# Optimization experiments

Measured on AMD Instinct MI355X. Metric: run time of the kernel, lower is better.

The kernel has to match this reference:

```python
import jax, jax.numpy as jnp
import numpy as np

BLOCK = 128  # fp8 block-quant block size (128, 128)


def dequant_block_fp8_weight(w, scale_inv):
    """w: [O, I] fp8-valued weights (stored as f32); scale_inv: [O//128, I//128].
    Dequant = per-(128,128)-block multiply by scale."""
    O, I = w.shape
    wb = w.reshape(O // BLOCK, BLOCK, I // BLOCK, BLOCK)
    wb = wb * scale_inv[:, None, :, None]
    return wb.reshape(O, I)


def setup_inputs() -> dict:
    key = jax.random.key(0)
    ks = jax.random.split(key, 7)
    H, F, T = 5120, 1536, 8192  # hidden, moe_intermediate, tokens
    x = jax.random.normal(ks[0], (T, H), dtype=jnp.float32)
    w_gate = jax.random.normal(ks[1], (F, H), dtype=jnp.float32)
    s_gate = jax.random.uniform(ks[2], (F // BLOCK, H // BLOCK), dtype=jnp.float32) * 0.01 + 1e-4
    w_up = jax.random.normal(ks[3], (F, H), dtype=jnp.float32)
    s_up = jax.random.uniform(ks[4], (F // BLOCK, H // BLOCK), dtype=jnp.float32) * 0.01 + 1e-4
    w_down = jax.random.normal(ks[5], (H, F), dtype=jnp.float32)
    s_down = jax.random.uniform(ks[6], (H // BLOCK, F // BLOCK), dtype=jnp.float32) * 0.01 + 1e-4
    return {"x": x, "w_gate": w_gate, "s_gate": s_gate, "w_up": w_up,
            "s_up": s_up, "w_down": w_down, "s_down": s_down}


def reference(x, w_gate, s_gate, w_up, s_up, w_down, s_down):
    # down_proj(silu(gate_proj(x)) * up_proj(x)), each Linear dequantizing
    # block-scaled fp8 weights first (bias=False everywhere).
    wg = dequant_block_fp8_weight(w_gate, s_gate).astype(x.dtype)
    wu = dequant_block_fp8_weight(w_up, s_up).astype(x.dtype)
    wd = dequant_block_fp8_weight(w_down, s_down).astype(x.dtype)
    gate = jnp.einsum('th,fh->tf', x, wg)  # [T, F]
    up = jnp.einsum('th,fh->tf', x, wu)    # [T, F]
    h = jax.nn.silu(gate) * up
    out = jnp.einsum('tf,hf->th', h, wd)   # [T, H]
    return out
```

## Files before the change

kernel.cpp:

```cpp
#include <hip/hip_runtime.h>


typedef __bf16 bf16x8 __attribute__((ext_vector_type(8)));
typedef float  f32x4  __attribute__((ext_vector_type(4)));
typedef unsigned int u32x4 __attribute__((ext_vector_type(4)));

__device__ __forceinline__ void glds16(const __bf16* g, __bf16* l) {
  __builtin_amdgcn_global_load_lds(
      (const __attribute__((address_space(1))) void*)g,
      (__attribute__((address_space(3))) void*)l, 16, 0, 0);
}

__device__ __forceinline__ void chunk_rk(int c, int& row, int& k) {
  int s = c >> 6;
  int w = (c & 63) << 4;
  int wl = w ^ (((w >> 9) & 1) << 5) ^ (((w >> 7) & 1) << 4);
  row = (s << 4) + (wl >> 6);
  k = (wl & 63) >> 1;
}

#define LGKM0()                                        \
  do {                                                 \
    asm volatile("s_waitcnt lgkmcnt(0)" ::: "memory"); \
    __builtin_amdgcn_sched_barrier(0);                 \
  } while (0)

#define VMBAR(n)                                                       \
  do {                                                                 \
    __builtin_amdgcn_sched_barrier(0);                                 \
    asm volatile("s_waitcnt vmcnt(" #n ")\n\ts_barrier" ::: "memory"); \
    __builtin_amdgcn_sched_barrier(0);                                 \
  } while (0)

__device__ __forceinline__ void cast8(const float* __restrict__ in,
                                      __bf16* __restrict__ out, size_t idx) {
  f32x4 a = *(const f32x4*)(in + idx);
  f32x4 b = *(const f32x4*)(in + idx + 4);
  bf16x8 o;
#pragma unroll
  for (int i = 0; i < 4; ++i) { o[i] = (__bf16)a[i]; o[i + 4] = (__bf16)b[i]; }
  *(bf16x8*)(out + idx) = o;
}

__global__ void prep(const float* __restrict__ x, const float* __restrict__ wg,
                     const float* __restrict__ sg, const float* __restrict__ wu,
                     const float* __restrict__ su, const float* __restrict__ wd,
                     const float* __restrict__ sd, __bf16* __restrict__ xb,
                     __bf16* __restrict__ wq, __bf16* __restrict__ wdq) {
  int bid = blockIdx.x;
  int tid = threadIdx.x;
  if (bid < 20480) {
    cast8(x, xb, ((size_t)bid * 256 + tid) * 8);
  } else if (bid < 28160) {
    unsigned g = (unsigned)(bid - 20480) * 256u + (unsigned)tid;
    unsigned lane = g & 63u, c = lane & 15u, q = lane >> 4;
    unsigned fr = (g >> 6) & 15u;
    unsigned u = g >> 10;
    unsigned bx = u / 160u;
    unsigned t = u - bx * 160u;
    unsigned nc = (bx << 8) | (fr << 4) | c;
    unsigned k = (t << 5) | (q << 3);
    unsigned f = nc >> 1;
    const float* wsrc = (nc & 1) ? wu : wg;
    const float* ssrc = (nc & 1) ? su : sg;
    float sc = ssrc[(f >> 7) * 40 + (k >> 7)];
    size_t si = (size_t)f * 5120 + k;
    f32x4 a = *(const f32x4*)(wsrc + si);
    f32x4 b = *(const f32x4*)(wsrc + si + 4);
    bf16x8 o;
#pragma unroll
    for (int i = 0; i < 4; ++i) {
      o[i] = (__bf16)(a[i] * sc);
      o[i + 4] = (__bf16)(b[i] * sc);
    }
    *(bf16x8*)(wq + (size_t)g * 8) = o;
  } else {
    unsigned g = (unsigned)(bid - 28160) * 256u + (unsigned)tid;
    unsigned lane = g & 63u, c = lane & 15u, q = lane >> 4;
    unsigned fr = (g >> 6) & 15u;
    unsigned u = g >> 10;
    unsigned bx = u / 48u;
    unsigned t = u - bx * 48u;
    unsigned nc = (bx << 8) | (fr << 4) | c;
    unsigned k = (t << 5) | (q << 3);
    float sc = sd[(nc >> 7) * 12 + (k >> 7)];
    size_t si = (size_t)nc * 1536 + k;
    f32x4 a = *(const f32x4*)(wd + si);
    f32x4 b = *(const f32x4*)(wd + si + 4);
    bf16x8 o;
#pragma unroll
    for (int i = 0; i < 4; ++i) {
      o[i] = (__bf16)(a[i] * sc);
      o[i + 4] = (__bf16)(b[i] * sc);
    }
    *(bf16x8*)(wdq + (size_t)g * 8) = o;
  }
}

template <bool FUSE_SILU, typename OutT>
__global__ __launch_bounds__(256, 2) void gemm_p(
    const __bf16* __restrict__ A, const __bf16* __restrict__ Bfm,
    OutT* __restrict__ C, int M, int N, int K, int ldc, int nbx) {
  __shared__ __bf16 lds[4 * 4096];
  const int tid = threadIdx.x;
  const int lane = tid & 63;
  const int wave = tid >> 6;
  const int lr = lane & 15;
  const int NT = K >> 5, NTm1 = NT - 1;

  const int nwg = gridDim.x;
  const int lb = (blockIdx.x & 7) * (nwg >> 3) + (blockIdx.x >> 3);
  const int bx = lb % nbx;
  const int by = lb / nbx;
  const int m0 = by * 128, n0 = bx * 256;

  int laneoff = (lr << 6) | ((lane >> 4) << 4);
  laneoff ^= ((lr & 2) << 3) | ((lr & 8) << 2);

  int r0, k0, r1, k1;
  chunk_rk(tid, r0, k0);
  chunk_rk(tid + 256, r1, k1);
  const unsigned o0 = (unsigned)r0 * K + (unsigned)k0;
  const unsigned o1 = (unsigned)r1 * K + (unsigned)k1;
  const int d0 = tid << 3, d1 = (tid + 256) << 3;
  const __bf16* Ab = A + (size_t)m0 * K;
  const __bf16* Bf =
      Bfm + ((size_t)bx * NT * 16 + wave * 4) * 512 + (size_t)lane * 8;

  f32x4 acc[8][4] = {};
  bf16x8 af[4];
  u32x4 bgA[4], bgB[4];

  auto STAGE_A = [&](int t_, int s_) {
    __bf16* lp = lds + s_ * 4096;
    const unsigned ko = (unsigned)t_ << 5;
    glds16(Ab + (o0 + ko), lp + d0);
    glds16(Ab + (o1 + ko), lp + d1);
  };
  auto RD_A = [&](const char* cb, int h) {
#pragma unroll
    for (int i = 0; i < 4; ++i)
      af[i] = *(const bf16x8*)(cb + (((h << 2) + i) << 10) + laneoff);
  };
  auto MFMA16 = [&](int h, u32x4 (&bk)[4]) {
    __builtin_amdgcn_s_setprio(1);
#pragma unroll
    for (int j = 0; j < 4; ++j) {
      bf16x8 b = __builtin_bit_cast(bf16x8, bk[j]);
#pragma unroll
      for (int i = 0; i < 4; ++i)
        acc[(h << 2) + i][j] = __builtin_amdgcn_mfma_f32_16x16x32_bf16(
            af[i], b, acc[(h << 2) + i][j], 0, 0, 0);
    }
    __builtin_amdgcn_s_setprio(0);
  };

#define B_LOAD(t_, B_)                                                       \
  {                                                                          \
    const __bf16* bp = Bf + (size_t)(t_) * 8192;                             \
    asm volatile("global_load_dwordx4 %0, %1, off" : "=v"(B_[0]) : "v"(bp)); \
    asm volatile("global_load_dwordx4 %0, %1, off offset:1024"               \
                 : "=v"(B_[1]) : "v"(bp));                                   \
    asm volatile("global_load_dwordx4 %0, %1, off offset:2048"               \
                 : "=v"(B_[2]) : "v"(bp));                                   \
    asm volatile("global_load_dwordx4 %0, %1, off offset:3072"               \
                 : "=v"(B_[3]) : "v"(bp));                                   \
  }

  STAGE_A(0, 0);
  B_LOAD(0, bgA);
  STAGE_A(1, 1);
  B_LOAD(1, bgB);

#define KSTEP(u_, B_)                                \
  {                                                  \
    int tn = t + (u_) + 2;                           \
    if (tn > NTm1) tn = NTm1;      \
    const char* cb = (const char*)lds + (u_) * 8192; \
    VMBAR(6);                                        \
    RD_A(cb, 0);                                     \
    STAGE_A(tn, ((u_) + 2) & 3);                     \
    LGKM0();                                         \
    MFMA16(0, B_);                                   \
    RD_A(cb, 1);                                     \
    LGKM0();                                         \
    MFMA16(1, B_);                                   \
    B_LOAD(tn, B_);                                  \
  }

  for (int t = 0; t < NT; t += 4) {
    KSTEP(0, bgA);
    KSTEP(1, bgB);
    KSTEP(2, bgA);
    KSTEP(3, bgB);
  }
  VMBAR(0);
#undef KSTEP
#undef B_LOAD

  const int colb = n0 + (wave << 6) + lr;
  const int rowb = m0 + ((lane >> 4) << 2);
#pragma unroll
  for (int i = 0; i < 8; ++i)
#pragma unroll
    for (int j = 0; j < 4; ++j)
#pragma unroll
      for (int r = 0; r < 4; ++r) {
        if constexpr (FUSE_SILU) {
          float v = acc[i][j][r];
          float p = __shfl_xor(v, 1, 64);
          float g = (lane & 1) ? p : v;
          float u = (lane & 1) ? v : p;
          float hv = (g / (1.0f + __expf(-g))) * u;
          if ((lane & 1) == 0)
            C[(size_t)(rowb + i * 16 + r) * ldc + ((colb + j * 16) >> 1)] =
                (OutT)hv;
        } else {
          C[(size_t)(rowb + i * 16 + r) * ldc + (colb + j * 16)] =
              (OutT)acc[i][j][r];
        }
      }
}

extern "C" void kernel_launch(void* const* d_in, const int* in_sizes, int n_in,
                              void* d_out, int out_size, void* d_ws,
                              size_t ws_size, hipStream_t stream) {
  const int Hd = 5120, Fd = 1536, Td = 8192;
  const float* x = (const float*)d_in[0];
  const float* wg = (const float*)d_in[1];
  const float* sg = (const float*)d_in[2];
  const float* wu = (const float*)d_in[3];
  const float* su = (const float*)d_in[4];
  const float* wd = (const float*)d_in[5];
  const float* sd = (const float*)d_in[6];
  float* out = (float*)d_out;

  __bf16* ws = (__bf16*)d_ws;
  const size_t xsz = (size_t)Td * Hd;
  __bf16* xb = ws;
  __bf16* wqf = xb + xsz;
  __bf16* wdqf = wqf + (size_t)2 * Fd * Hd;
  __bf16* hbuf = wdqf + (size_t)Hd * Fd;

  prep<<<32000, 256, 0, stream>>>(x, wg, sg, wu, su, wd, sd, xb, wqf, wdqf);

  gemm_p<true, __bf16><<<768, 256, 0, stream>>>(xb, wqf, hbuf, Td, 2 * Fd, Hd,
                                                Fd, 12);

  gemm_p<false, float><<<1280, 256, 0, stream>>>(hbuf, wdqf, out, Td, Hd, Fd,
                                                 Hd, 20);
}
```

Measured before the change: 698.3 us.

## Restructure GEMM main loop to 64-wide K steps with 3-stage LDS ring

The GEMM main loop now processes 64 K-elements per iteration instead of 32. It uses a triple-buffered LDS ring of 64-wide A tiles and double-buffered A fragment registers, so LDS reads for the next half overlap MFMA issue through partial lgkmcnt waits. This halves the number of vmcnt+s_barrier synchronisations per K and is meant to keep the matrix cores fed more continuously. In exchange it uses more LDS (48KB vs 32KB) and more registers, which may threaten the 2-blocks-per-CU occupancy, and the B prefetch distance changes.

```diff
diff --git a/kernel.cpp b/kernel.cpp
--- a/kernel.cpp
+++ b/kernel.cpp
@@ -19,10 +19,10 @@
   k = (wl & 63) >> 1;
 }
 
-#define LGKM0()                                        \
-  do {                                                 \
-    asm volatile("s_waitcnt lgkmcnt(0)" ::: "memory"); \
-    __builtin_amdgcn_sched_barrier(0);                 \
+#define LGKMC(n)                                              \
+  do {                                                        \
+    asm volatile("s_waitcnt lgkmcnt(" #n ")" ::: "memory");   \
+    __builtin_amdgcn_sched_barrier(0);                        \
   } while (0)
 
 #define VMBAR(n)                                                       \
@@ -101,12 +101,13 @@
 __global__ __launch_bounds__(256, 2) void gemm_p(
     const __bf16* __restrict__ A, const __bf16* __restrict__ Bfm,
     OutT* __restrict__ C, int M, int N, int K, int ldc, int nbx) {
-  __shared__ __bf16 lds[4 * 4096];
+  __shared__ __bf16 lds[3 * 8192];
   const int tid = threadIdx.x;
   const int lane = tid & 63;
   const int wave = tid >> 6;
   const int lr = lane & 15;
-  const int NT = K >> 5, NTm1 = NT - 1;
+  const int NT = K >> 5;
+  const int NS = K >> 6;
 
   const int nwg = gridDim.x;
   const int lb = (blockIdx.x & 7) * (nwg >> 3) + (blockIdx.x >> 3);
@@ -128,36 +129,40 @@
       Bfm + ((size_t)bx * NT * 16 + wave * 4) * 512 + (size_t)lane * 8;
 
   f32x4 acc[8][4] = {};
-  bf16x8 af[4];
+  bf16x8 af0[4], af1[4];
   u32x4 bgA[4], bgB[4];
 
   auto STAGE_A = [&](int t_, int s_) {
-    __bf16* lp = lds + s_ * 4096;
-    const unsigned ko = (unsigned)t_ << 5;
-    glds16(Ab + (o0 + ko), lp + d0);
-    glds16(Ab + (o1 + ko), lp + d1);
+    __bf16* lp = lds + s_ * 8192;
+#pragma unroll
+    for (int ks = 0; ks < 2; ++ks) {
+      const unsigned ko = ((unsigned)t_ << 6) | (ks << 5);
+      glds16(Ab + (o0 + ko), lp + ks * 4096 + d0);
+      glds16(Ab + (o1 + ko), lp + ks * 4096 + d1);
+    }
   };
-  auto RD_A = [&](const char* cb, int h) {
-#pragma unroll
-    for (int i = 0; i < 4; ++i)
-      af[i] = *(const bf16x8*)(cb + (((h << 2) + i) << 10) + laneoff);
-  };
-  auto MFMA16 = [&](int h, u32x4 (&bk)[4]) {
-    __builtin_amdgcn_s_setprio(1);
-#pragma unroll
-    for (int j = 0; j < 4; ++j) {
-      bf16x8 b = __builtin_bit_cast(bf16x8, bk[j]);
-#pragma unroll
-      for (int i = 0; i < 4; ++i)
-        acc[(h << 2) + i][j] = __builtin_amdgcn_mfma_f32_16x16x32_bf16(
-            af[i], b, acc[(h << 2) + i][j], 0, 0, 0);
-    }
-    __builtin_amdgcn_s_setprio(0);
-  };
-
-#define B_LOAD(t_, B_)                                                       \
+
+#define RD4(dst_, base_, h_)                                              \
+  {                                                                       \
+    _Pragma("unroll") for (int i = 0; i < 4; ++i) dst_[i] =               \
+        *(const bf16x8*)((base_) + ((((h_) << 2) + i) << 10) + laneoff);  \
+  }
+
+#define MFMA16(h_, af_, bk_)                                              \
+  {                                                                       \
+    __builtin_amdgcn_s_setprio(1);                                        \
+    _Pragma("unroll") for (int j = 0; j < 4; ++j) {                       \
+      bf16x8 b_ = __builtin_bit_cast(bf16x8, bk_[j]);                     \
+      _Pragma("unroll") for (int i = 0; i < 4; ++i)                       \
+          acc[((h_) << 2) + i][j] = __builtin_amdgcn_mfma_f32_16x16x32_bf16( \
+              af_[i], b_, acc[((h_) << 2) + i][j], 0, 0, 0);              \
+    }                                                                     \
+    __builtin_amdgcn_s_setprio(0);                                        \
+  }
+
+#define B_LOAD(t32_, B_)                                                     \
   {                                                                          \
-    const __bf16* bp = Bf + (size_t)(t_) * 8192;                             \
+    const __bf16* bp = Bf + (size_t)(t32_) * 8192;                           \
     asm volatile("global_load_dwordx4 %0, %1, off" : "=v"(B_[0]) : "v"(bp)); \
     asm volatile("global_load_dwordx4 %0, %1, off offset:1024"               \
                  : "=v"(B_[1]) : "v"(bp));                                   \
@@ -169,33 +174,37 @@
 
   STAGE_A(0, 0);
   B_LOAD(0, bgA);
+  B_LOAD(1, bgB);
   STAGE_A(1, 1);
-  B_LOAD(1, bgB);
-
-#define KSTEP(u_, B_)                                \
-  {                                                  \
-    int tn = t + (u_) + 2;                           \
-    if (tn > NTm1) tn = NTm1;      \
-    const char* cb = (const char*)lds + (u_) * 8192; \
-    VMBAR(6);                                        \
-    RD_A(cb, 0);                                     \
-    STAGE_A(tn, ((u_) + 2) & 3);                     \
-    LGKM0();                                         \
-    MFMA16(0, B_);                                   \
-    RD_A(cb, 1);                                     \
-    LGKM0();                                         \
-    MFMA16(1, B_);                                   \
-    B_LOAD(tn, B_);                                  \
-  }
-
-  for (int t = 0; t < NT; t += 4) {
-    KSTEP(0, bgA);
-    KSTEP(1, bgB);
-    KSTEP(2, bgA);
-    KSTEP(3, bgB);
+  VMBAR(4);
+
+  int cur = 0, stg = 2;
+  for (int t = 0; t < NS; ++t) {
+    const char* cb = (const char*)lds + cur * 16384;
+    int tn = t + 2; if (tn > NS - 1) tn = NS - 1;
+    int tb = t + 1; if (tb > NS - 1) tb = NS - 1;
+    RD4(af0, cb, 0);
+    RD4(af1, cb, 1);
+    LGKMC(4);
+    MFMA16(0, af0, bgA);
+    LGKMC(0);
+    RD4(af0, cb + 8192, 0);
+    MFMA16(1, af1, bgA);
+    B_LOAD(2 * tb, bgA);
+    RD4(af1, cb + 8192, 1);
+    LGKMC(4);
+    MFMA16(0, af0, bgB);
+    LGKMC(0);
+    MFMA16(1, af1, bgB);
+    B_LOAD(2 * tb + 1, bgB);
+    STAGE_A(tn, stg);
+    VMBAR(4);
+    cur = (cur == 2) ? 0 : cur + 1;
+    stg = (stg == 2) ? 0 : stg + 1;
   }
   VMBAR(0);
-#undef KSTEP
+#undef RD4
+#undef MFMA16
 #undef B_LOAD
 
   const int colb = n0 + (wave << 6) + lr;
```

After: 717.9 us. +2.8%, slower.
